# Performance work log

Measured on AMD Instinct MI355X. Metric: run time of the kernel, lower is better.

Reference implementation:

```python
import jax, jax.numpy as jnp
import numpy as np

N_NODES = 50000
N_EDGES = 800000
D_IN = 96
D_OUT = 96


def setup_inputs() -> dict:
    key = jax.random.key(0)
    k1, k2, k3, k4, k5 = jax.random.split(key, 5)
    x = jax.random.normal(k1, (N_NODES, D_IN), dtype=jnp.float32)
    edge_w = jax.random.uniform(k2, (N_EDGES,), dtype=jnp.float32)
    weight = jax.random.normal(k3, (D_IN, D_OUT), dtype=jnp.float32) * (1.0 / np.sqrt(D_IN))
    bias = jnp.zeros((D_OUT,), dtype=jnp.float32)
    row = jax.random.randint(k4, (N_EDGES,), 0, N_NODES, dtype=jnp.int32)
    col = jax.random.randint(k5, (N_EDGES,), 0, N_NODES, dtype=jnp.int32)
    return {"x": x, "edge_w": edge_w, "weight": weight, "bias": bias, "row": row, "col": col}


def reference(x, edge_w, weight, bias, row, col):
    # hidden_hat = support @ x, with support given in COO form (row, col, edge_w)
    # gather source-node features, scale by edge weight, scatter-add to destination
    msgs = edge_w[:, None] * x[col]                      # [E, D_in]
    hidden_hat = jax.ops.segment_sum(msgs, row, num_segments=N_NODES)  # [N, D_in]
    # hidden_tilde = hidden_hat @ W + b
    hidden_tilde = jnp.dot(hidden_hat, weight) + bias    # [N, D_out]
    return jax.nn.relu(hidden_tilde)
```

## Files before the change

### kernel.cpp

```cpp
#include <hip/hip_runtime.h>
#include <hip/hip_fp16.h>

#define N_NODES 50000
#define N_EDGES 800000
#define D 96
#define D4 (D / 4)

#define BIN_SH 6
#define BIN_NODES 64
#define NBINS 782
#define MAXB 1536

#define TBLOCKS 782
#define SBLOCKS 392
#define EPB 2041
#define WT_LD 104

typedef _Float16 f16x8 __attribute__((ext_vector_type(8)));
typedef float    f32x4 __attribute__((ext_vector_type(4)));

__global__ __launch_bounds__(256) void transform_scatter(
        const float* __restrict__ x, const float* __restrict__ W,
        const int* __restrict__ row, const int* __restrict__ col,
        const float* __restrict__ edge_w,
        __half* __restrict__ y, int* __restrict__ cursor,
        int2* __restrict__ binned) {
    __shared__ __align__(16) int smem[5000];
    const int t = threadIdx.x;
    const int bid = blockIdx.x;

    if (bid >= TBLOCKS) {
        int* lh    = smem;
        int* gbase = smem + NBINS;
        int* lcur  = smem + 2 * NBINS;
        for (int i = t; i < NBINS; i += 256) { lh[i] = 0; lcur[i] = 0; }
        __syncthreads();
        int e0 = (bid - TBLOCKS) * EPB;
        int e1 = min(e0 + EPB, N_EDGES);
        for (int e = e0 + t; e < e1; e += 256)
            atomicAdd(&lh[row[e] >> BIN_SH], 1);
        __syncthreads();
        for (int i = t; i < NBINS; i += 256)
            gbase[i] = lh[i] ? (i * MAXB + atomicAdd(&cursor[i], lh[i])) : 0;
        __syncthreads();
        for (int e = e0 + t; e < e1; e += 256) {
            int r = row[e];
            int b = r >> BIN_SH;
            int p = atomicAdd(&lcur[b], 1);
            binned[gbase[b] + p] = make_int2(col[e] | ((r & 63) << 16),
                                             __float_as_int(edge_w[e]));
        }
        return;
    }

    _Float16* WT = reinterpret_cast<_Float16*>(smem);
    for (int i = t; i < D * D; i += 256) {
        int k = i / D, n2 = i % D;
        WT[n2 * WT_LD + k] = (_Float16)W[i];
    }
    __syncthreads();

    const int lane = t & 63;
    const int wv   = t >> 6;
    const int wid  = bid * 4 + wv;
    const int n0   = wid * 16;
    if (n0 >= N_NODES) return;

    const int arow = lane & 15;
    const int kgrp = lane >> 4;

    const float4* xr = reinterpret_cast<const float4*>(x) +
                       (long long)(n0 + arow) * D4;
    f16x8 afrag[3];
    #pragma unroll
    for (int ks = 0; ks < 3; ++ks) {
        float4 v0 = xr[ks * 8 + kgrp * 2];
        float4 v1 = xr[ks * 8 + kgrp * 2 + 1];
        f16x8 a;
        a[0] = (_Float16)v0.x; a[1] = (_Float16)v0.y;
        a[2] = (_Float16)v0.z; a[3] = (_Float16)v0.w;
        a[4] = (_Float16)v1.x; a[5] = (_Float16)v1.y;
        a[6] = (_Float16)v1.z; a[7] = (_Float16)v1.w;
        afrag[ks] = a;
    }

    const int bcol = lane & 15;
    #pragma unroll
    for (int nt = 0; nt < 6; ++nt) {
        f32x4 acc = {0.f, 0.f, 0.f, 0.f};
        #pragma unroll
        for (int ks = 0; ks < 3; ++ks) {
            f16x8 b = *reinterpret_cast<const f16x8*>(
                &WT[(nt * 16 + bcol) * WT_LD + ks * 32 + kgrp * 8]);
            acc = __builtin_amdgcn_mfma_f32_16x16x32_f16(afrag[ks], b, acc, 0, 0, 0);
        }
        #pragma unroll
        for (int i = 0; i < 4; ++i) {
            int rrow = kgrp * 4 + i;
            y[(long long)(n0 + rrow) * D + nt * 16 + bcol] = __float2half_rn(acc[i]);
        }
    }
}

__global__ __launch_bounds__(384) void binsort_aggregate(
        const int* __restrict__ cursor, const int2* __restrict__ binned,
        const __half* __restrict__ y, const float* __restrict__ bias,
        float* __restrict__ out) {
    __shared__ int2 recs[MAXB];
    __shared__ int hist[BIN_NODES];
    __shared__ int sc[BIN_NODES];
    __shared__ int lcur[BIN_NODES];
    __shared__ int nodeoff[BIN_NODES + 1];
    int t = threadIdx.x;
    int b = blockIdx.x;
    int base = b * MAXB;
    int size = cursor[b];
    if (size > MAXB) size = MAXB;
    if (t < BIN_NODES) hist[t] = 0;
    __syncthreads();

    int2 rl0, rl1, rl2, rl3;
    int i0 = t, i1 = t + 384, i2 = t + 768, i3 = t + 1152;
    if (i0 < size) { rl0 = binned[base + i0]; atomicAdd(&hist[(rl0.x >> 16) & 63], 1); }
    if (i1 < size) { rl1 = binned[base + i1]; atomicAdd(&hist[(rl1.x >> 16) & 63], 1); }
    if (i2 < size) { rl2 = binned[base + i2]; atomicAdd(&hist[(rl2.x >> 16) & 63], 1); }
    if (i3 < size) { rl3 = binned[base + i3]; atomicAdd(&hist[(rl3.x >> 16) & 63], 1); }
    __syncthreads();

    int h = 0;
    if (t < BIN_NODES) { h = hist[t]; sc[t] = h; }
    for (int off = 1; off < BIN_NODES; off <<= 1) {
        __syncthreads();
        int a = (t >= off && t < BIN_NODES) ? sc[t - off] : 0;
        __syncthreads();
        if (t < BIN_NODES) sc[t] += a;
    }
    __syncthreads();
    if (t < BIN_NODES) { int excl = sc[t] - h; nodeoff[t] = excl; lcur[t] = excl; }
    if (t == 0) nodeoff[BIN_NODES] = size;
    __syncthreads();

    if (i0 < size) { int lr = (rl0.x >> 16) & 63; int p = atomicAdd(&lcur[lr], 1);
                     recs[p] = make_int2(rl0.x & 0xFFFF, rl0.y); }
    if (i1 < size) { int lr = (rl1.x >> 16) & 63; int p = atomicAdd(&lcur[lr], 1);
                     recs[p] = make_int2(rl1.x & 0xFFFF, rl1.y); }
    if (i2 < size) { int lr = (rl2.x >> 16) & 63; int p = atomicAdd(&lcur[lr], 1);
                     recs[p] = make_int2(rl2.x & 0xFFFF, rl2.y); }
    if (i3 < size) { int lr = (rl3.x >> 16) & 63; int p = atomicAdd(&lcur[lr], 1);
                     recs[p] = make_int2(rl3.x & 0xFFFF, rl3.y); }
    __syncthreads();

    const uint4* yu = reinterpret_cast<const uint4*>(y);
    int c  = t % 12;
    int gg = t / 12;
    #pragma unroll
    for (int pass = 0; pass < 2; ++pass) {
        int g = pass * 32 + gg;
        int n = (b << BIN_SH) + g;
        if (n < N_NODES) {
            int beg = nodeoff[g];
            int end = nodeoff[g + 1];
            float acc[8];
            #pragma unroll
            for (int i = 0; i < 8; ++i) acc[i] = 0.0f;
            for (int j = beg; j < end; ++j) {
                int2 rec = recs[j];
                float w = __int_as_float(rec.y);
                uint4 v = yu[(long long)rec.x * 12 + c];
                float2 f0 = __half22float2(*reinterpret_cast<const __half2*>(&v.x));
                float2 f1 = __half22float2(*reinterpret_cast<const __half2*>(&v.y));
                float2 f2 = __half22float2(*reinterpret_cast<const __half2*>(&v.z));
                float2 f3 = __half22float2(*reinterpret_cast<const __half2*>(&v.w));
                acc[0] = fmaf(w, f0.x, acc[0]);
                acc[1] = fmaf(w, f0.y, acc[1]);
                acc[2] = fmaf(w, f1.x, acc[2]);
                acc[3] = fmaf(w, f1.y, acc[3]);
                acc[4] = fmaf(w, f2.x, acc[4]);
                acc[5] = fmaf(w, f2.y, acc[5]);
                acc[6] = fmaf(w, f3.x, acc[6]);
                acc[7] = fmaf(w, f3.y, acc[7]);
            }
            const float4* b4 = reinterpret_cast<const float4*>(bias);
            float4 ba = b4[c * 2], bb = b4[c * 2 + 1];
            float4 o0, o1;
            o0.x = fmaxf(acc[0] + ba.x, 0.f);
            o0.y = fmaxf(acc[1] + ba.y, 0.f);
            o0.z = fmaxf(acc[2] + ba.z, 0.f);
            o0.w = fmaxf(acc[3] + ba.w, 0.f);
            o1.x = fmaxf(acc[4] + bb.x, 0.f);
            o1.y = fmaxf(acc[5] + bb.y, 0.f);
            o1.z = fmaxf(acc[6] + bb.z, 0.f);
            o1.w = fmaxf(acc[7] + bb.w, 0.f);
            float4* op = reinterpret_cast<float4*>(&out[(long long)n * D + c * 8]);
            op[0] = o0;
            op[1] = o1;
        }
    }
}

__global__ void zero_f32(float* __restrict__ p, long long n) {
    long long i = (long long)blockIdx.x * blockDim.x + threadIdx.x;
    long long stride = (long long)gridDim.x * blockDim.x;
    for (; i < n; i += stride) p[i] = 0.0f;
}

__global__ __launch_bounds__(256) void scatter_edges(
        const float* __restrict__ x, const float* __restrict__ edge_w,
        const int* __restrict__ row, const int* __restrict__ col,
        float* __restrict__ hidden) {
    long long t = (long long)blockIdx.x * blockDim.x + threadIdx.x;
    const long long total = (long long)N_EDGES * D4;
    if (t >= total) return;
    int e = (int)(t / D4);
    int c = (int)(t % D4);
    float w = edge_w[e];
    const float4 v = *reinterpret_cast<const float4*>(&x[(long long)col[e] * D + c * 4]);
    float* o = &hidden[(long long)row[e] * D + c * 4];
    atomicAdd(o + 0, w * v.x);
    atomicAdd(o + 1, w * v.y);
    atomicAdd(o + 2, w * v.z);
    atomicAdd(o + 3, w * v.w);
}

__global__ __launch_bounds__(256) void gemm_bias_relu(
        const float* __restrict__ hidden, const float* __restrict__ W,
        const float* __restrict__ bias, float* __restrict__ out) {
    __shared__ float Ws[D * D];
    __shared__ float bs[D];
    for (int i = threadIdx.x; i < D * D; i += blockDim.x) Ws[i] = W[i];
    if (threadIdx.x < D) bs[threadIdx.x] = bias[threadIdx.x];
    __syncthreads();
    const long long total = (long long)N_NODES * D;
    long long stride = (long long)gridDim.x * blockDim.x;
    for (long long idx = (long long)blockIdx.x * blockDim.x + threadIdx.x;
         idx < total; idx += stride) {
        int n = (int)(idx / D);
        int d = (int)(idx % D);
        const float* hrow = &hidden[(long long)n * D];
        float acc = bs[d];
        #pragma unroll
        for (int k = 0; k < D; ++k) acc = fmaf(hrow[k], Ws[k * D + d], acc);
        out[idx] = fmaxf(acc, 0.0f);
    }
}

extern "C" void kernel_launch(void* const* d_in, const int* in_sizes, int n_in,
                              void* d_out, int out_size, void* d_ws, size_t ws_size,
                              hipStream_t stream) {
    const float* x      = (const float*)d_in[0];
    const float* edge_w = (const float*)d_in[1];
    const float* weight = (const float*)d_in[2];
    const float* bias   = (const float*)d_in[3];
    const int*   row    = (const int*)d_in[4];
    const int*   col    = (const int*)d_in[5];
    float* out = (float*)d_out;

    const size_t yBytes      = (size_t)N_NODES * D * sizeof(__half);
    const size_t binnedBytes = (size_t)NBINS * MAXB * sizeof(int2);
    const size_t curBytes    = (size_t)NBINS * sizeof(int);
    const size_t need = yBytes + binnedBytes + curBytes + 64;

    if (ws_size >= need) {
        char* wsb = (char*)d_ws;
        __half* y      = (__half*)wsb; wsb += yBytes;
        int2*   binned = (int2*)wsb;   wsb += binnedBytes;
        int*    cursor = (int*)wsb;

        hipMemsetAsync(cursor, 0, curBytes, stream);
        transform_scatter<<<TBLOCKS + SBLOCKS, 256, 0, stream>>>(
            x, weight, row, col, edge_w, y, cursor, binned);
        binsort_aggregate<<<NBINS, 384, 0, stream>>>(cursor, binned, y, bias, out);
    } else {
        float* hidden = (float*)d_ws;
        const long long hidden_elems = (long long)N_NODES * D;
        zero_f32<<<2048, 256, 0, stream>>>(hidden, hidden_elems);
        long long total = (long long)N_EDGES * D4;
        scatter_edges<<<(int)((total + 255) / 256), 256, 0, stream>>>(x, edge_w, row,
                                                                      col, hidden);
        gemm_bias_relu<<<2048, 256, 0, stream>>>(hidden, weight, bias, out);
    }
}
```

Before: 67.97 us.

## Widen aggregate blocks to one node per thread group, unroll gather by two

The binsort_aggregate kernel moves to 768 threads so each 12-thread group handles one node in a single pass, replacing two sequential passes. The per-node gather loop is unrolled by two with separate accumulators, so two independent y loads are in flight at once. Separately, the scatter phase of transform_scatter uses half as many blocks, each handling twice as many edges. The aim is more memory-level parallelism in the gather. In exchange, each block uses more registers and threads, which can lower occupancy, and the scatter phase has fewer blocks.

```diff
diff --git a/kernel.cpp b/kernel.cpp
--- a/kernel.cpp
+++ b/kernel.cpp
@@ -12,8 +12,8 @@
 #define MAXB 1536
 
 #define TBLOCKS 782
-#define SBLOCKS 392
-#define EPB 2041
+#define SBLOCKS 196
+#define EPB 4082
 #define WT_LD 104
 
 typedef _Float16 f16x8 __attribute__((ext_vector_type(8)));
@@ -102,7 +102,7 @@
     }
 }
 
-__global__ __launch_bounds__(384) void binsort_aggregate(
+__global__ __launch_bounds__(768) void binsort_aggregate(
         const int* __restrict__ cursor, const int2* __restrict__ binned,
         const __half* __restrict__ y, const float* __restrict__ bias,
         float* __restrict__ out) {
@@ -119,12 +119,10 @@
     if (t < BIN_NODES) hist[t] = 0;
     __syncthreads();
 
-    int2 rl0, rl1, rl2, rl3;
-    int i0 = t, i1 = t + 384, i2 = t + 768, i3 = t + 1152;
+    int2 rl0, rl1;
+    int i0 = t, i1 = t + 768;
     if (i0 < size) { rl0 = binned[base + i0]; atomicAdd(&hist[(rl0.x >> 16) & 63], 1); }
     if (i1 < size) { rl1 = binned[base + i1]; atomicAdd(&hist[(rl1.x >> 16) & 63], 1); }
-    if (i2 < size) { rl2 = binned[base + i2]; atomicAdd(&hist[(rl2.x >> 16) & 63], 1); }
-    if (i3 < size) { rl3 = binned[base + i3]; atomicAdd(&hist[(rl3.x >> 16) & 63], 1); }
     __syncthreads();
 
     int h = 0;
@@ -144,58 +142,87 @@
                      recs[p] = make_int2(rl0.x & 0xFFFF, rl0.y); }
     if (i1 < size) { int lr = (rl1.x >> 16) & 63; int p = atomicAdd(&lcur[lr], 1);
                      recs[p] = make_int2(rl1.x & 0xFFFF, rl1.y); }
-    if (i2 < size) { int lr = (rl2.x >> 16) & 63; int p = atomicAdd(&lcur[lr], 1);
-                     recs[p] = make_int2(rl2.x & 0xFFFF, rl2.y); }
-    if (i3 < size) { int lr = (rl3.x >> 16) & 63; int p = atomicAdd(&lcur[lr], 1);
-                     recs[p] = make_int2(rl3.x & 0xFFFF, rl3.y); }
     __syncthreads();
 
     const uint4* yu = reinterpret_cast<const uint4*>(y);
-    int c  = t % 12;
-    int gg = t / 12;
+    int c = t % 12;
+    int g = t / 12;
+    int n = (b << BIN_SH) + g;
+    if (n >= N_NODES) return;
+    int beg = nodeoff[g];
+    int end = nodeoff[g + 1];
+
+    float acc[8], acc2[8];
     #pragma unroll
-    for (int pass = 0; pass < 2; ++pass) {
-        int g = pass * 32 + gg;
-        int n = (b << BIN_SH) + g;
-        if (n < N_NODES) {
-            int beg = nodeoff[g];
-            int end = nodeoff[g + 1];
-            float acc[8];
-            #pragma unroll
-            for (int i = 0; i < 8; ++i) acc[i] = 0.0f;
-            for (int j = beg; j < end; ++j) {
-                int2 rec = recs[j];
-                float w = __int_as_float(rec.y);
-                uint4 v = yu[(long long)rec.x * 12 + c];
-                float2 f0 = __half22float2(*reinterpret_cast<const __half2*>(&v.x));
-                float2 f1 = __half22float2(*reinterpret_cast<const __half2*>(&v.y));
-                float2 f2 = __half22float2(*reinterpret_cast<const __half2*>(&v.z));
-                float2 f3 = __half22float2(*reinterpret_cast<const __half2*>(&v.w));
-                acc[0] = fmaf(w, f0.x, acc[0]);
-                acc[1] = fmaf(w, f0.y, acc[1]);
-                acc[2] = fmaf(w, f1.x, acc[2]);
-                acc[3] = fmaf(w, f1.y, acc[3]);
-                acc[4] = fmaf(w, f2.x, acc[4]);
-                acc[5] = fmaf(w, f2.y, acc[5]);
-                acc[6] = fmaf(w, f3.x, acc[6]);
-                acc[7] = fmaf(w, f3.y, acc[7]);
-            }
-            const float4* b4 = reinterpret_cast<const float4*>(bias);
-            float4 ba = b4[c * 2], bb = b4[c * 2 + 1];
-            float4 o0, o1;
-            o0.x = fmaxf(acc[0] + ba.x, 0.f);
-            o0.y = fmaxf(acc[1] + ba.y, 0.f);
-            o0.z = fmaxf(acc[2] + ba.z, 0.f);
-            o0.w = fmaxf(acc[3] + ba.w, 0.f);
-            o1.x = fmaxf(acc[4] + bb.x, 0.f);
-            o1.y = fmaxf(acc[5] + bb.y, 0.f);
-            o1.z = fmaxf(acc[6] + bb.z, 0.f);
-            o1.w = fmaxf(acc[7] + bb.w, 0.f);
-            float4* op = reinterpret_cast<float4*>(&out[(long long)n * D + c * 8]);
-            op[0] = o0;
-            op[1] = o1;
-        }
-    }
+    for (int i = 0; i < 8; ++i) { acc[i] = 0.0f; acc2[i] = 0.0f; }
+
+    int j = beg;
+    for (; j + 1 < end; j += 2) {
+        int2 r0 = recs[j];
+        int2 r1 = recs[j + 1];
+        float w0 = __int_as_float(r0.y);
+        float w1 = __int_as_float(r1.y);
+        uint4 v0 = yu[(long long)r0.x * 12 + c];
+        uint4 v1 = yu[(long long)r1.x * 12 + c];
+        float2 a0 = __half22float2(*reinterpret_cast<const __half2*>(&v0.x));
+        float2 a1 = __half22float2(*reinterpret_cast<const __half2*>(&v0.y));
+        float2 a2 = __half22float2(*reinterpret_cast<const __half2*>(&v0.z));
+        float2 a3 = __half22float2(*reinterpret_cast<const __half2*>(&v0.w));
+        acc[0] = fmaf(w0, a0.x, acc[0]);
+        acc[1] = fmaf(w0, a0.y, acc[1]);
+        acc[2] = fmaf(w0, a1.x, acc[2]);
+        acc[3] = fmaf(w0, a1.y, acc[3]);
+        acc[4] = fmaf(w0, a2.x, acc[4]);
+        acc[5] = fmaf(w0, a2.y, acc[5]);
+        acc[6] = fmaf(w0, a3.x, acc[6]);
+        acc[7] = fmaf(w0, a3.y, acc[7]);
+        float2 b0 = __half22float2(*reinterpret_cast<const __half2*>(&v1.x));
+        float2 b1 = __half22float2(*reinterpret_cast<const __half2*>(&v1.y));
+        float2 b2 = __half22float2(*reinterpret_cast<const __half2*>(&v1.z));
+        float2 b3 = __half22float2(*reinterpret_cast<const __half2*>(&v1.w));
+        acc2[0] = fmaf(w1, b0.x, acc2[0]);
+        acc2[1] = fmaf(w1, b0.y, acc2[1]);
+        acc2[2] = fmaf(w1, b1.x, acc2[2]);
+        acc2[3] = fmaf(w1, b1.y, acc2[3]);
+        acc2[4] = fmaf(w1, b2.x, acc2[4]);
+        acc2[5] = fmaf(w1, b2.y, acc2[5]);
+        acc2[6] = fmaf(w1, b3.x, acc2[6]);
+        acc2[7] = fmaf(w1, b3.y, acc2[7]);
+    }
+    if (j < end) {
+        int2 r0 = recs[j];
+        float w0 = __int_as_float(r0.y);
+        uint4 v0 = yu[(long long)r0.x * 12 + c];
+        float2 a0 = __half22float2(*reinterpret_cast<const __half2*>(&v0.x));
+        float2 a1 = __half22float2(*reinterpret_cast<const __half2*>(&v0.y));
+        float2 a2 = __half22float2(*reinterpret_cast<const __half2*>(&v0.z));
+        float2 a3 = __half22float2(*reinterpret_cast<const __half2*>(&v0.w));
+        acc[0] = fmaf(w0, a0.x, acc[0]);
+        acc[1] = fmaf(w0, a0.y, acc[1]);
+        acc[2] = fmaf(w0, a1.x, acc[2]);
+        acc[3] = fmaf(w0, a1.y, acc[3]);
+        acc[4] = fmaf(w0, a2.x, acc[4]);
+        acc[5] = fmaf(w0, a2.y, acc[5]);
+        acc[6] = fmaf(w0, a3.x, acc[6]);
+        acc[7] = fmaf(w0, a3.y, acc[7]);
+    }
+    #pragma unroll
+    for (int i = 0; i < 8; ++i) acc[i] += acc2[i];
+
+    const float4* b4 = reinterpret_cast<const float4*>(bias);
+    float4 ba = b4[c * 2], bb = b4[c * 2 + 1];
+    float4 o0, o1;
+    o0.x = fmaxf(acc[0] + ba.x, 0.f);
+    o0.y = fmaxf(acc[1] + ba.y, 0.f);
+    o0.z = fmaxf(acc[2] + ba.z, 0.f);
+    o0.w = fmaxf(acc[3] + ba.w, 0.f);
+    o1.x = fmaxf(acc[4] + bb.x, 0.f);
+    o1.y = fmaxf(acc[5] + bb.y, 0.f);
+    o1.z = fmaxf(acc[6] + bb.z, 0.f);
+    o1.w = fmaxf(acc[7] + bb.w, 0.f);
+    float4* op = reinterpret_cast<float4*>(&out[(long long)n * D + c * 8]);
+    op[0] = o0;
+    op[1] = o1;
 }
 
 __global__ void zero_f32(float* __restrict__ p, long long n) {
@@ -269,7 +296,7 @@
         hipMemsetAsync(cursor, 0, curBytes, stream);
         transform_scatter<<<TBLOCKS + SBLOCKS, 256, 0, stream>>>(
             x, weight, row, col, edge_w, y, cursor, binned);
-        binsort_aggregate<<<NBINS, 384, 0, stream>>>(cursor, binned, y, bias, out);
+        binsort_aggregate<<<NBINS, 768, 0, stream>>>(cursor, binned, y, bias, out);
     } else {
         float* hidden = (float*)d_ws;
         const long long hidden_elems = (long long)N_NODES * D;
```

New measurement: 66.38 us. 1.02x faster.
